# Optimization experiments

Hardware: AMD Instinct MI355X
Metric: run time of the kernel (lower is better)

## Reference

```python
import jax, jax.numpy as jnp
import numpy as np

HID = 256
EDGE_F = 64
N_CELL = 4096
N_EDGE = 65536
BSZ = 4
EPS = 1e-5


def setup_inputs() -> dict:
    key = jax.random.key(0)
    ks = jax.random.split(key, 12)
    def lin(k, fan_in, fan_out):
        # torch Linear default init: U(-1/sqrt(fan_in), 1/sqrt(fan_in))
        bound = 1.0 / np.sqrt(fan_in)
        kw, kb = jax.random.split(k)
        W = jax.random.uniform(kw, (fan_in, fan_out), jnp.float32, -bound, bound)
        b = jax.random.uniform(kb, (fan_out,), jnp.float32, -bound, bound)
        return W, b
    cell_x = jax.random.normal(ks[0], (BSZ, N_CELL, HID), jnp.float32)
    edge_index = jax.random.randint(ks[1], (BSZ, N_EDGE, 2), 0, N_CELL, jnp.int64)
    edge_attr = jax.random.normal(ks[2], (BSZ, N_EDGE, EDGE_F), jnp.float32)
    mW1, mb1 = lin(ks[3], HID + EDGE_F, HID)
    mW2, mb2 = lin(ks[4], HID, HID)
    uW1, ub1 = lin(ks[5], 2 * HID, HID)
    uW2, ub2 = lin(ks[6], HID, HID)
    gamma = jnp.ones((HID,), jnp.float32)
    beta = jnp.zeros((HID,), jnp.float32)
    return {"cell_x": cell_x, "edge_index": edge_index, "edge_attr": edge_attr,
            "mW1": mW1, "mb1": mb1, "mW2": mW2, "mb2": mb2,
            "uW1": uW1, "ub1": ub1, "uW2": uW2, "ub2": ub2,
            "gamma": gamma, "beta": beta}


def reference(cell_x, edge_index, edge_attr, mW1, mb1, mW2, mb2,
              uW1, ub1, uW2, ub2, gamma, beta):
    n_cell = cell_x.shape[1]
    src = jnp.clip(edge_index[..., 0], 0, n_cell - 1)  # [B, E]
    dst = jnp.clip(edge_index[..., 1], 0, n_cell - 1)  # [B, E]

    # gather source node features per edge: [B, E, H]
    src_x = jnp.take_along_axis(cell_x, src[..., None], axis=1)

    # edge message MLP
    m_in = jnp.concatenate([src_x, edge_attr], axis=-1)  # [B, E, H+F]
    msg = jax.nn.relu(m_in @ mW1 + mb1) @ mW2 + mb2      # [B, E, H]

    # mean aggregation at destination nodes (scatter-add + count)
    def agg_one(m, d):
        s = jax.ops.segment_sum(m, d, num_segments=n_cell)                    # [N, H]
        c = jax.ops.segment_sum(jnp.ones((d.shape[0],), m.dtype), d,
                                num_segments=n_cell)                          # [N]
        return s / jnp.maximum(c, 1.0)[:, None]
    agg = jax.vmap(agg_one)(msg, dst)  # [B, N, H]

    # node update MLP + residual LayerNorm
    u_in = jnp.concatenate([cell_x, agg], axis=-1)        # [B, N, 2H]
    out = jax.nn.relu(u_in @ uW1 + ub1) @ uW2 + ub2       # [B, N, H]
    h = cell_x + out
    mu = jnp.mean(h, axis=-1, keepdims=True)
    var = jnp.mean(jnp.square(h - mu), axis=-1, keepdims=True)
    return (h - mu) * jax.lax.rsqrt(var + EPS) * gamma + beta
```

## Files before the change

kernel.cpp:

```cpp
#include <hip/hip_runtime.h>
#include <hip/hip_bf16.h>

#define HID 256
#define EF  64
#define KIN 320
#define NC  4096
#define NE  65536
#define BSZ 4
#define EPSV 1e-5f

typedef unsigned short ushort_t;
typedef __attribute__((ext_vector_type(8))) short s16x8;
typedef __attribute__((ext_vector_type(16))) float f32x16;

#define EPAD 68
#define HPAD 260
#define UPAD 520
#define HSF  260

__device__ __forceinline__ ushort_t bf16_rne(float f) {
    unsigned u = __float_as_uint(f);
    return (ushort_t)((u + 0x7fffu + ((u >> 16) & 1u)) >> 16);
}
__device__ __forceinline__ float bf16_to_f(ushort_t u) {
    return __uint_as_float(((unsigned)u) << 16);
}
__device__ __forceinline__ unsigned pk_bf16(float a, float b) {
    __hip_bfloat162 h = __float22bfloat162_rn(make_float2(a, b));
    return *reinterpret_cast<unsigned*>(&h);
}
__device__ __forceinline__ void split_bf16(float v, ushort_t& h, ushort_t& l) {
    unsigned u = __float_as_uint(v);
    h = (ushort_t)(u >> 16);
    float hf = __uint_as_float(u & 0xffff0000u);
    l = (ushort_t)(__float_as_uint(v - hf) >> 16);
}

__device__ __forceinline__ void pack_one(const float* W, int idx,
                                         ushort_t* hi, ushort_t* lo) {
    int l = idx & 63;
    int tn = idx >> 6;
    int nt = tn & 7, t = tn >> 3;
    int k0 = t * 16 + (l >> 5) * 8;
    int col = nt * 32 + (l & 31);
    #pragma unroll
    for (int j = 0; j < 8; ++j) {
        float v = W[(size_t)(k0 + j) * 256 + col];
        ushort_t h, lw;
        split_bf16(v, h, lw);
        hi[(size_t)idx * 8 + j] = h;
        lo[(size_t)idx * 8 + j] = lw;
    }
}

#define FR1 10240
#define FR2 8192
#define PACK1B 104
#define FUSEB 256
#define ZEROB 256

__global__ __launch_bounds__(256)
void prep_kernel(const float* __restrict__ mW1, const float* __restrict__ uW1,
                 const float* __restrict__ uW2, const float* __restrict__ mW2,
                 const float* __restrict__ ub1, const float* __restrict__ mb2,
                 ushort_t* __restrict__ w1hi, ushort_t* __restrict__ w1lo,
                 ushort_t* __restrict__ u1hi, ushort_t* __restrict__ u1lo,
                 ushort_t* __restrict__ u2hi, ushort_t* __restrict__ u2lo,
                 float* __restrict__ W2u, float* __restrict__ bias2u,
                 float4* __restrict__ zp, int n4) {
    int bid = blockIdx.x;
    if (bid < PACK1B) {
        int idx = bid * 256 + threadIdx.x;
        if (idx < FR1) { pack_one(mW1, idx, w1hi, w1lo); return; }
        idx -= FR1;
        if (idx < FR2) { pack_one(uW1, idx, u1hi, u1lo); return; }
        idx -= FR2;
        pack_one(uW2, idx, u2hi, u2lo);
        return;
    }
    bid -= PACK1B;
    if (bid < FUSEB) {
        int k = bid, n = threadIdx.x;
        const float* wrow = mW2 + (size_t)k * 256;
        float acc = 0.f;
        #pragma unroll 8
        for (int m = 0; m < 256; ++m)
            acc = fmaf(wrow[m], uW1[(size_t)(256 + m) * 256 + n], acc);
        W2u[(size_t)k * 256 + n] = acc;
        return;
    }
    bid -= FUSEB;
    if (bid == 0) {
        int n = threadIdx.x;
        float acc = ub1[n];
        #pragma unroll 8
        for (int m = 0; m < 256; ++m)
            acc = fmaf(mb2[m], uW1[(size_t)(256 + m) * 256 + n], acc);
        bias2u[n] = acc;
        return;
    }
    bid -= 1;
    int i = bid * 256 + threadIdx.x;
    int stride = ZEROB * 256;
    float4 z = make_float4(0.f, 0.f, 0.f, 0.f);
    for (; i < n4; i += stride) zp[i] = z;
}

__global__ __launch_bounds__(512, 4)
void hp_kernel(const int* __restrict__ eidx, float* __restrict__ counts,
               const float* __restrict__ cell_x,
               const ushort_t* __restrict__ w1hi, const ushort_t* __restrict__ w1lo,
               const ushort_t* __restrict__ u1hi, const ushort_t* __restrict__ u1lo,
               float* __restrict__ Pe, ushort_t* __restrict__ Pn,
               const float* __restrict__ W2u,
               ushort_t* __restrict__ w2uhi, ushort_t* __restrict__ w2ulo) {
    __shared__ ushort_t Us[32 * HPAD];

    if (blockIdx.x < 512) {
        int i = blockIdx.x * 512 + threadIdx.x;
        int b = i >> 16;
        int2 v = ((const int2*)eidx)[i];
        int d = min(max(v.y, 0), NC - 1);
        atomicAdd(&counts[b * NC + d], 1.0f);
        return;
    }
    if (blockIdx.x >= 1024) {
        int idx = (blockIdx.x - 1024) * 512 + threadIdx.x;
        pack_one(W2u, idx, w2uhi, w2ulo);
        return;
    }

    const int tid = threadIdx.x;
    const size_t r0 = (size_t)(blockIdx.x - 512) * 32;
    const int wv = tid >> 6, ln = tid & 63;
    const int m32 = ln & 31, half = ln >> 5;
    const int col = wv * 32 + m32;

    const ushort_t* wph = w1hi + ((size_t)wv * 64 + ln) * 8;
    const ushort_t* wpl = w1lo + ((size_t)wv * 64 + ln) * 8;
    const ushort_t* uph = u1hi + ((size_t)wv * 64 + ln) * 8;
    const ushort_t* upl = u1lo + ((size_t)wv * 64 + ln) * 8;
    s16x8 wh = *(const s16x8*)wph, wl = *(const s16x8*)wpl;
    s16x8 uh = *(const s16x8*)uph, ul = *(const s16x8*)upl;

    {
        const int row = tid >> 4, c8 = tid & 15;
        const float4* crow = (const float4*)(cell_x + (r0 + row) * HID);
        #pragma unroll
        for (int i = 0; i < 4; ++i) {
            int c = c8 + i * 16;
            float4 v = crow[c];
            *(uint2*)&Us[row * HPAD + c * 4] =
                make_uint2(pk_bf16(v.x, v.y), pk_bf16(v.z, v.w));
        }
    }
    __syncthreads();

    f32x16 aw, au;
    #pragma unroll
    for (int r = 0; r < 16; ++r) { aw[r] = 0.f; au[r] = 0.f; }

    #pragma unroll 2
    for (int t = 0; t < 16; ++t) {
        int tn = (t + 1 < 16) ? t + 1 : 15;
        s16x8 whn = *(const s16x8*)(wph + (size_t)tn * 4096);
        s16x8 wln = *(const s16x8*)(wpl + (size_t)tn * 4096);
        s16x8 uhn = *(const s16x8*)(uph + (size_t)tn * 4096);
        s16x8 uln = *(const s16x8*)(upl + (size_t)tn * 4096);
        s16x8 a = *(const s16x8*)&Us[m32 * HPAD + t * 16 + half * 8];
        aw = __builtin_amdgcn_mfma_f32_32x32x16_bf16(a, wh, aw, 0, 0, 0);
        aw = __builtin_amdgcn_mfma_f32_32x32x16_bf16(a, wl, aw, 0, 0, 0);
        au = __builtin_amdgcn_mfma_f32_32x32x16_bf16(a, uh, au, 0, 0, 0);
        au = __builtin_amdgcn_mfma_f32_32x32x16_bf16(a, ul, au, 0, 0, 0);
        wh = whn; wl = wln; uh = uhn; ul = uln;
    }

    #pragma unroll
    for (int r = 0; r < 16; ++r) {
        int row = (r & 3) + 8 * (r >> 2) + 4 * half;
        Pe[(r0 + row) * 256 + col] = aw[r];
        Pn[(r0 + row) * 256 + col] = bf16_rne(au[r]);
    }
}

__global__ __launch_bounds__(512, 4)
void scansc_kernel(const int* __restrict__ eidx, const float* __restrict__ counts,
                   int* __restrict__ filled, int* __restrict__ sorted) {
    __shared__ int woffL[NC];
    __shared__ int wsum[8];

    const int t = threadIdx.x;
    const int b = blockIdx.x >> 7;

    int c[8];
    int ts = 0;
    const int base = b * NC + t * 8;
    #pragma unroll
    for (int j = 0; j < 8; ++j) { c[j] = (int)counts[base + j]; ts += c[j]; }

    int lane = t & 63;
    int x = ts;
    #pragma unroll
    for (int off = 1; off < 64; off <<= 1) {
        int y = __shfl_up(x, off, 64);
        if (lane >= off) x += y;
    }
    if (lane == 63) wsum[t >> 6] = x;
    __syncthreads();
    if (t == 0) {
        int s = 0;
        #pragma unroll
        for (int w = 0; w < 8; ++w) { int tmp = wsum[w]; wsum[w] = s; s += tmp; }
    }
    __syncthreads();
    int run = wsum[t >> 6] + (x - ts);
    #pragma unroll
    for (int j = 0; j < 8; ++j) { woffL[t * 8 + j] = run; run += c[j]; }
    __syncthreads();

    int e = (blockIdx.x & 127) * 512 + t;
    int2 v = ((const int2*)eidx)[(size_t)b * NE + e];
    int d = min(max(v.y, 0), NC - 1);
    int pos = woffL[d] + atomicAdd(&filled[b * NC + d], 1);
    sorted[(size_t)b * NE + pos] = e;
}

__global__ __launch_bounds__(512, 4)
void edge_kernel(const float* __restrict__ Pe,
                 const int*   __restrict__ eidx,
                 const int*   __restrict__ sorted,
                 const float* __restrict__ eattr,
                 const ushort_t* __restrict__ w1hi, const ushort_t* __restrict__ w1lo,
                 const float* __restrict__ b1,
                 float* __restrict__ aggf) {
    __shared__ ushort_t Xs[64 * EPAD];

    const int tid = threadIdx.x;
    const int b   = blockIdx.x >> 10;
    const int e0  = (blockIdx.x & 1023) * 64;
    const int wv = tid >> 6, ln = tid & 63;
    const int m32 = ln & 31, half = ln >> 5;
    const int col = wv * 32 + m32;

    int eid = sorted[(size_t)b * NE + e0 + ln];
    int2 ev = ((const int2*)eidx)[(size_t)b * NE + eid];
    int src = min(max(ev.x, 0), NC - 1);
    int dst = min(max(ev.y, 0), NC - 1);

    const ushort_t* ph = w1hi + ((size_t)(16 * 8 + wv) * 64 + ln) * 8;
    const ushort_t* pl = w1lo + ((size_t)(16 * 8 + wv) * 64 + ln) * 8;
    s16x8 bh0 = *(const s16x8*)ph;
    s16x8 bl0 = *(const s16x8*)pl;
    s16x8 bh1 = *(const s16x8*)(ph + 4096);
    s16x8 bl1 = *(const s16x8*)(pl + 4096);
    s16x8 bh2 = *(const s16x8*)(ph + 8192);
    s16x8 bl2 = *(const s16x8*)(pl + 8192);
    s16x8 bh3 = *(const s16x8*)(ph + 12288);
    s16x8 bl3 = *(const s16x8*)(pl + 12288);

    float t0[16], t1[16];
    {
        const float* pb = Pe + (size_t)b * NC * 256 + col;
        #pragma unroll
        for (int r = 0; r < 16; ++r) {
            int rw = (r & 3) + 8 * (r >> 2) + 4 * half;
            t0[r] = pb[(size_t)__shfl(src, rw, 64) * 256];
            t1[r] = pb[(size_t)__shfl(src, rw + 32, 64) * 256];
        }
    }

    {
        const int rowE = tid >> 3, c8 = tid & 7;
        int eidr = __shfl(eid, rowE, 64);
        const float4* arow = (const float4*)(eattr + ((size_t)b * NE + eidr) * EF);
        #pragma unroll
        for (int i = 0; i < 2; ++i) {
            int c = c8 + i * 8;
            float4 v = arow[c];
            *(uint2*)&Xs[rowE * EPAD + c * 4] =
                make_uint2(pk_bf16(v.x, v.y), pk_bf16(v.z, v.w));
        }
    }
    __syncthreads();

    f32x16 A0, A1;
    {
        float bias = b1[col];
        #pragma unroll
        for (int r = 0; r < 16; ++r) { A0[r] = bias; A1[r] = bias; }
    }
    {
        int ao = m32 * EPAD + half * 8;
        s16x8 a0, a1;
        a0 = *(const s16x8*)&Xs[ao];      a1 = *(const s16x8*)&Xs[ao + 32 * EPAD];
        A0 = __builtin_amdgcn_mfma_f32_32x32x16_bf16(a0, bh0, A0, 0, 0, 0);
        A0 = __builtin_amdgcn_mfma_f32_32x32x16_bf16(a0, bl0, A0, 0, 0, 0);
        A1 = __builtin_amdgcn_mfma_f32_32x32x16_bf16(a1, bh0, A1, 0, 0, 0);
        A1 = __builtin_amdgcn_mfma_f32_32x32x16_bf16(a1, bl0, A1, 0, 0, 0);
        a0 = *(const s16x8*)&Xs[ao + 16]; a1 = *(const s16x8*)&Xs[ao + 16 + 32 * EPAD];
        A0 = __builtin_amdgcn_mfma_f32_32x32x16_bf16(a0, bh1, A0, 0, 0, 0);
        A0 = __builtin_amdgcn_mfma_f32_32x32x16_bf16(a0, bl1, A0, 0, 0, 0);
        A1 = __builtin_amdgcn_mfma_f32_32x32x16_bf16(a1, bh1, A1, 0, 0, 0);
        A1 = __builtin_amdgcn_mfma_f32_32x32x16_bf16(a1, bl1, A1, 0, 0, 0);
        a0 = *(const s16x8*)&Xs[ao + 32]; a1 = *(const s16x8*)&Xs[ao + 32 + 32 * EPAD];
        A0 = __builtin_amdgcn_mfma_f32_32x32x16_bf16(a0, bh2, A0, 0, 0, 0);
        A0 = __builtin_amdgcn_mfma_f32_32x32x16_bf16(a0, bl2, A0, 0, 0, 0);
        A1 = __builtin_amdgcn_mfma_f32_32x32x16_bf16(a1, bh2, A1, 0, 0, 0);
        A1 = __builtin_amdgcn_mfma_f32_32x32x16_bf16(a1, bl2, A1, 0, 0, 0);
        a0 = *(const s16x8*)&Xs[ao + 48]; a1 = *(const s16x8*)&Xs[ao + 48 + 32 * EPAD];
        A0 = __builtin_amdgcn_mfma_f32_32x32x16_bf16(a0, bh3, A0, 0, 0, 0);
        A0 = __builtin_amdgcn_mfma_f32_32x32x16_bf16(a0, bl3, A0, 0, 0, 0);
        A1 = __builtin_amdgcn_mfma_f32_32x32x16_bf16(a1, bh3, A1, 0, 0, 0);
        A1 = __builtin_amdgcn_mfma_f32_32x32x16_bf16(a1, bl3, A1, 0, 0, 0);
    }

    #pragma unroll
    for (int r = 0; r < 16; ++r) {
        A0[r] = fmaxf(A0[r] + t0[r], 0.f);
        A1[r] = fmaxf(A1[r] + t1[r], 0.f);
    }

    {
        const int l31 = ln & 31;
        int dl = __shfl(dst, l31, 64);
        int dp = __shfl(dst, (l31 == 0) ? 0 : l31 - 1, 64);
        if (l31 == 0) dp = ~dl;
        unsigned m = (unsigned)__ballot(dl != dp);
        unsigned rem = m & ~1u;
        float prev = (((A0[0] + A0[1]) + (A0[2] + A0[3])) + ((A0[4] + A0[5]) + (A0[6] + A0[7])))
                   + (((A0[8] + A0[9]) + (A0[10] + A0[11])) + ((A0[12] + A0[13]) + (A0[14] + A0[15])));
        int lo = 0;
        while (lo < 32) {
            int hi = rem ? (int)__builtin_ctz(rem) : 32;
            rem &= rem - 1;
            int d = __shfl(dl, lo, 64);
            float shi = 0.f;
            if (hi < 32) {
                #pragma unroll
                for (int r = 0; r < 16; ++r) {
                    int row = (r & 3) + 8 * (r >> 2) + 4 * half;
                    shi += (row >= hi) ? A0[r] : 0.f;
                }
            }
            float s = prev - shi;
            prev = shi;
            s += __shfl_xor(s, 32, 64);
            if (ln < 32) atomicAdd(&aggf[((size_t)b * NC + d) * HID + col], s);
            lo = hi;
        }
        dl = __shfl(dst, 32 + l31, 64);
        dp = __shfl(dst, 32 + ((l31 == 0) ? 0 : l31 - 1), 64);
        if (l31 == 0) dp = ~dl;
        m = (unsigned)__ballot(dl != dp);
        rem = m & ~1u;
        prev = (((A1[0] + A1[1]) + (A1[2] + A1[3])) + ((A1[4] + A1[5]) + (A1[6] + A1[7])))
             + (((A1[8] + A1[9]) + (A1[10] + A1[11])) + ((A1[12] + A1[13]) + (A1[14] + A1[15])));
        lo = 0;
        while (lo < 32) {
            int hi = rem ? (int)__builtin_ctz(rem) : 32;
            rem &= rem - 1;
            int d = __shfl(dl, lo, 64);
            float shi = 0.f;
            if (hi < 32) {
                #pragma unroll
                for (int r = 0; r < 16; ++r) {
                    int row = (r & 3) + 8 * (r >> 2) + 4 * half;
                    shi += (row >= hi) ? A1[r] : 0.f;
                }
            }
            float s = prev - shi;
            prev = shi;
            s += __shfl_xor(s, 32, 64);
            if (ln < 32) atomicAdd(&aggf[((size_t)b * NC + d) * HID + col], s);
            lo = hi;
        }
    }
}

__global__ __launch_bounds__(512, 6)
void node_kernel(const float* __restrict__ cell_x,
                 const float* __restrict__ aggf,
                 const float* __restrict__ counts,
                 const ushort_t* __restrict__ Pn,
                 const ushort_t* __restrict__ w2uhi, const ushort_t* __restrict__ w2ulo,
                 const float* __restrict__ bias2u,
                 const ushort_t* __restrict__ u2hi, const ushort_t* __restrict__ u2lo,
                 const float* __restrict__ b2,
                 const float* __restrict__ gamma, const float* __restrict__ beta,
                 float* __restrict__ out) {
    __shared__ ushort_t Us[32 * UPAD];
    float* hs = (float*)Us;

    const int tid = threadIdx.x;
    const int b   = blockIdx.x >> 7;
    const int r0  = (blockIdx.x & 127) * 32;
    const int wv = tid >> 6, ln = tid & 63;
    const int m32 = ln & 31, half = ln >> 5;
    const int col = wv * 32 + m32;

    const ushort_t* b1ph = w2uhi + ((size_t)wv * 64 + ln) * 8;
    const ushort_t* b1pl = w2ulo + ((size_t)wv * 64 + ln) * 8;
    s16x8 bhi = *(const s16x8*)b1ph;
    s16x8 blo = *(const s16x8*)b1pl;

    ushort_t pnt[16];
    {
        const ushort_t* pb = Pn + ((size_t)b * NC + r0) * 256 + col;
        #pragma unroll
        for (int r = 0; r < 16; ++r) {
            int row = (r & 3) + 8 * (r >> 2) + 4 * half;
            pnt[r] = pb[(size_t)row * 256];
        }
    }

    {
        const int row = tid >> 4, c8 = tid & 15;
        float inv = 1.0f / fmaxf(counts[b * NC + r0 + row], 1.0f);
        const float4* grow = (const float4*)(aggf + ((size_t)b * NC + r0 + row) * HID);
        #pragma unroll
        for (int i = 0; i < 4; ++i) {
            int c = c8 + i * 16;
            float4 g = grow[c];
            *(uint2*)&Us[row * HPAD + c * 4] =
                make_uint2(pk_bf16(g.x * inv, g.y * inv), pk_bf16(g.z * inv, g.w * inv));
        }
    }
    __syncthreads();

    f32x16 acc;
    {
        float bias = bias2u[col];
        #pragma unroll
        for (int r = 0; r < 16; ++r) acc[r] = bias;
    }
    #pragma unroll 2
    for (int t = 0; t < 16; ++t) {
        int tn1 = (t + 1 < 16) ? t + 1 : 15;
        s16x8 bhin = *(const s16x8*)(b1ph + (size_t)tn1 * 4096);
        s16x8 blon = *(const s16x8*)(b1pl + (size_t)tn1 * 4096);
        s16x8 a = *(const s16x8*)&Us[m32 * HPAD + t * 16 + half * 8];
        acc = __builtin_amdgcn_mfma_f32_32x32x16_bf16(a, bhi, acc, 0, 0, 0);
        acc = __builtin_amdgcn_mfma_f32_32x32x16_bf16(a, blo, acc, 0, 0, 0);
        bhi = bhin; blo = blon;
    }

    #pragma unroll
    for (int r = 0; r < 16; ++r) acc[r] += bf16_to_f(pnt[r]);

    const ushort_t* b2ph = u2hi + ((size_t)wv * 64 + ln) * 8;
    const ushort_t* b2pl = u2lo + ((size_t)wv * 64 + ln) * 8;
    bhi = *(const s16x8*)b2ph;
    blo = *(const s16x8*)b2pl;

    __syncthreads();

    #pragma unroll
    for (int r = 0; r < 16; ++r) {
        int row = (r & 3) + 8 * (r >> 2) + 4 * half;
        Us[row * HPAD + col] = bf16_rne(fmaxf(acc[r], 0.f));
    }
    __syncthreads();

    float cxt[16];
    #pragma unroll
    for (int r = 0; r < 16; ++r) {
        int row = (r & 3) + 8 * (r >> 2) + 4 * half;
        cxt[r] = cell_x[((size_t)b * NC + r0 + row) * HID + col];
    }

    f32x16 c2;
    {
        float bias = b2[col];
        #pragma unroll
        for (int r = 0; r < 16; ++r) c2[r] = bias;
    }
    #pragma unroll 2
    for (int t = 0; t < 16; ++t) {
        int tn1 = (t + 1 < 16) ? t + 1 : 15;
        s16x8 bhin = *(const s16x8*)(b2ph + (size_t)tn1 * 4096);
        s16x8 blon = *(const s16x8*)(b2pl + (size_t)tn1 * 4096);
        s16x8 a = *(const s16x8*)&Us[m32 * HPAD + t * 16 + half * 8];
        c2 = __builtin_amdgcn_mfma_f32_32x32x16_bf16(a, bhi, c2, 0, 0, 0);
        c2 = __builtin_amdgcn_mfma_f32_32x32x16_bf16(a, blo, c2, 0, 0, 0);
        bhi = bhin; blo = blon;
    }
    __syncthreads();

    #pragma unroll
    for (int r = 0; r < 16; ++r) {
        int row = (r & 3) + 8 * (r >> 2) + 4 * half;
        hs[row * HSF + col] = c2[r] + cxt[r];
    }
    __syncthreads();

    #pragma unroll
    for (int i = 0; i < 4; ++i) {
        int r = wv * 4 + i;
        float v[4];
        float s = 0.f, q = 0.f;
        #pragma unroll
        for (int j = 0; j < 4; ++j) {
            v[j] = hs[r * HSF + ln + 64 * j];
            s += v[j];
            q = fmaf(v[j], v[j], q);
        }
        #pragma unroll
        for (int off = 32; off > 0; off >>= 1) {
            s += __shfl_xor(s, off, 64);
            q += __shfl_xor(q, off, 64);
        }
        float mu = s * (1.0f / HID);
        float var = q * (1.0f / HID) - mu * mu;
        float rs = rsqrtf(var + EPSV);
        float* orow = out + ((size_t)b * NC + r0 + r) * HID;
        #pragma unroll
        for (int j = 0; j < 4; ++j) {
            int c = ln + 64 * j;
            orow[c] = (v[j] - mu) * rs * gamma[c] + beta[c];
        }
    }
}

extern "C" void kernel_launch(void* const* d_in, const int* in_sizes, int n_in,
                              void* d_out, int out_size, void* d_ws, size_t ws_size,
                              hipStream_t stream) {
    const float* cell_x = (const float*)d_in[0];
    const int*   eidx   = (const int*)d_in[1];
    const float* eattr  = (const float*)d_in[2];
    const float* mW1    = (const float*)d_in[3];
    const float* mb1    = (const float*)d_in[4];
    const float* mW2    = (const float*)d_in[5];
    const float* mb2    = (const float*)d_in[6];
    const float* uW1    = (const float*)d_in[7];
    const float* ub1    = (const float*)d_in[8];
    const float* uW2    = (const float*)d_in[9];
    const float* ub2    = (const float*)d_in[10];
    const float* gamma  = (const float*)d_in[11];
    const float* beta   = (const float*)d_in[12];
    float* out = (float*)d_out;

    float* aggf   = (float*)d_ws;
    float* counts = aggf + (size_t)BSZ * NC * HID;
    int*   filled = (int*)(counts + BSZ * NC);
    int*   sorted = filled + BSZ * NC;
    ushort_t* w1hi = (ushort_t*)(sorted + (size_t)BSZ * NE);
    ushort_t* w1lo = w1hi + KIN * HID;
    ushort_t* u1hi = w1lo + KIN * HID;
    ushort_t* u1lo = u1hi + HID * HID;
    ushort_t* u2hi = u1lo + HID * HID;
    ushort_t* u2lo = u2hi + HID * HID;
    ushort_t* w2uhi = u2lo + HID * HID;
    ushort_t* w2ulo = w2uhi + HID * HID;
    float*    W2u   = (float*)(w2ulo + HID * HID);
    float*    bias2u = W2u + HID * HID;
    float*    Pe   = bias2u + HID;
    ushort_t* Pn   = (ushort_t*)(Pe + (size_t)BSZ * NC * 256);

    int n4 = (BSZ * NC * HID * 4 + BSZ * NC * 4 + BSZ * NC * 4) / 16;
    prep_kernel<<<PACK1B + FUSEB + 1 + ZEROB, 256, 0, stream>>>(
        mW1, uW1, uW2, mW2, ub1, mb2,
        w1hi, w1lo, u1hi, u1lo, u2hi, u2lo, W2u, bias2u, (float4*)d_ws, n4);
    hp_kernel<<<1040, 512, 0, stream>>>(eidx, counts, cell_x,
                                        w1hi, w1lo, u1hi, u1lo, Pe, Pn,
                                        W2u, w2uhi, w2ulo);
    scansc_kernel<<<512, 512, 0, stream>>>(eidx, counts, filled, sorted);
    edge_kernel<<<BSZ * NE / 64, 512, 0, stream>>>(Pe, eidx, sorted, eattr,
                                                   w1hi, w1lo, mb1, aggf);
    node_kernel<<<BSZ * NC / 32, 512, 0, stream>>>(cell_x, aggf, counts, Pn,
                                                   w2uhi, w2ulo, bias2u,
                                                   u2hi, u2lo, ub2,
                                                   gamma, beta, out);
}
```

Measured before the change: 251.2 us.

## Fold scan-scatter into hp kernel, move histogram to prep, use memset

Measured after the change: 249.0 us. No clear change (-0.9%).

```diff
diff --git a/kernel.cpp b/kernel.cpp
--- a/kernel.cpp
+++ b/kernel.cpp
@@ -17,6 +17,7 @@
 #define HPAD 260
 #define UPAD 520
 #define HSF  260
+#define HOFF 8320
 
 __device__ __forceinline__ ushort_t bf16_rne(float f) {
     unsigned u = __float_as_uint(f);
@@ -57,7 +58,7 @@
 #define FR2 8192
 #define PACK1B 104
 #define FUSEB 256
-#define ZEROB 256
+#define HISTB 1024
 
 __global__ __launch_bounds__(256)
 void prep_kernel(const float* __restrict__ mW1, const float* __restrict__ uW1,
@@ -67,7 +68,7 @@
                  ushort_t* __restrict__ u1hi, ushort_t* __restrict__ u1lo,
                  ushort_t* __restrict__ u2hi, ushort_t* __restrict__ u2lo,
                  float* __restrict__ W2u, float* __restrict__ bias2u,
-                 float4* __restrict__ zp, int n4) {
+                 const int* __restrict__ eidx, float* __restrict__ counts) {
     int bid = blockIdx.x;
     if (bid < PACK1B) {
         int idx = bid * 256 + threadIdx.x;
@@ -101,13 +102,15 @@
     }
     bid -= 1;
     int i = bid * 256 + threadIdx.x;
-    int stride = ZEROB * 256;
-    float4 z = make_float4(0.f, 0.f, 0.f, 0.f);
-    for (; i < n4; i += stride) zp[i] = z;
+    int b = i >> 16;
+    int2 v = ((const int2*)eidx)[i];
+    int d = min(max(v.y, 0), NC - 1);
+    atomicAdd(&counts[b * NC + d], 1.0f);
 }
 
 __global__ __launch_bounds__(512, 4)
-void hp_kernel(const int* __restrict__ eidx, float* __restrict__ counts,
+void hp_kernel(const int* __restrict__ eidx, const float* __restrict__ counts,
+               int* __restrict__ filled, int* __restrict__ sorted,
                const float* __restrict__ cell_x,
                const ushort_t* __restrict__ w1hi, const ushort_t* __restrict__ w1lo,
                const ushort_t* __restrict__ u1hi, const ushort_t* __restrict__ u1lo,
@@ -115,23 +118,56 @@
                const float* __restrict__ W2u,
                ushort_t* __restrict__ w2uhi, ushort_t* __restrict__ w2ulo) {
     __shared__ ushort_t Us[32 * HPAD];
-
-    if (blockIdx.x < 512) {
-        int i = blockIdx.x * 512 + threadIdx.x;
-        int b = i >> 16;
-        int2 v = ((const int2*)eidx)[i];
-        int d = min(max(v.y, 0), NC - 1);
-        atomicAdd(&counts[b * NC + d], 1.0f);
-        return;
-    }
+    __shared__ int wsum[8];
+
     if (blockIdx.x >= 1024) {
         int idx = (blockIdx.x - 1024) * 512 + threadIdx.x;
         pack_one(W2u, idx, w2uhi, w2ulo);
         return;
     }
 
+    if (blockIdx.x >= 512) {
+        int* woffL = (int*)Us;
+        const int t = threadIdx.x;
+        const int sbid = blockIdx.x - 512;
+        const int b = sbid >> 7;
+
+        int c[8];
+        int ts = 0;
+        const int base = b * NC + t * 8;
+        #pragma unroll
+        for (int j = 0; j < 8; ++j) { c[j] = (int)counts[base + j]; ts += c[j]; }
+
+        int lane = t & 63;
+        int x = ts;
+        #pragma unroll
+        for (int off = 1; off < 64; off <<= 1) {
+            int y = __shfl_up(x, off, 64);
+            if (lane >= off) x += y;
+        }
+        if (lane == 63) wsum[t >> 6] = x;
+        __syncthreads();
+        if (t == 0) {
+            int s = 0;
+            #pragma unroll
+            for (int w = 0; w < 8; ++w) { int tmp = wsum[w]; wsum[w] = s; s += tmp; }
+        }
+        __syncthreads();
+        int run = wsum[t >> 6] + (x - ts);
+        #pragma unroll
+        for (int j = 0; j < 8; ++j) { woffL[t * 8 + j] = run; run += c[j]; }
+        __syncthreads();
+
+        int e = (sbid & 127) * 512 + t;
+        int2 v = ((const int2*)eidx)[(size_t)b * NE + e];
+        int d = min(max(v.y, 0), NC - 1);
+        int pos = woffL[d] + atomicAdd(&filled[b * NC + d], 1);
+        sorted[(size_t)b * NE + pos] = e;
+        return;
+    }
+
     const int tid = threadIdx.x;
-    const size_t r0 = (size_t)(blockIdx.x - 512) * 32;
+    const size_t r0 = (size_t)blockIdx.x * 32;
     const int wv = tid >> 6, ln = tid & 63;
     const int m32 = ln & 31, half = ln >> 5;
     const int col = wv * 32 + m32;
@@ -181,48 +217,6 @@
         Pe[(r0 + row) * 256 + col] = aw[r];
         Pn[(r0 + row) * 256 + col] = bf16_rne(au[r]);
     }
-}
-
-__global__ __launch_bounds__(512, 4)
-void scansc_kernel(const int* __restrict__ eidx, const float* __restrict__ counts,
-                   int* __restrict__ filled, int* __restrict__ sorted) {
-    __shared__ int woffL[NC];
-    __shared__ int wsum[8];
-
-    const int t = threadIdx.x;
-    const int b = blockIdx.x >> 7;
-
-    int c[8];
-    int ts = 0;
-    const int base = b * NC + t * 8;
-    #pragma unroll
-    for (int j = 0; j < 8; ++j) { c[j] = (int)counts[base + j]; ts += c[j]; }
-
-    int lane = t & 63;
-    int x = ts;
-    #pragma unroll
-    for (int off = 1; off < 64; off <<= 1) {
-        int y = __shfl_up(x, off, 64);
-        if (lane >= off) x += y;
-    }
-    if (lane == 63) wsum[t >> 6] = x;
-    __syncthreads();
-    if (t == 0) {
-        int s = 0;
-        #pragma unroll
-        for (int w = 0; w < 8; ++w) { int tmp = wsum[w]; wsum[w] = s; s += tmp; }
-    }
-    __syncthreads();
-    int run = wsum[t >> 6] + (x - ts);
-    #pragma unroll
-    for (int j = 0; j < 8; ++j) { woffL[t * 8 + j] = run; run += c[j]; }
-    __syncthreads();
-
-    int e = (blockIdx.x & 127) * 512 + t;
-    int2 v = ((const int2*)eidx)[(size_t)b * NE + e];
-    int d = min(max(v.y, 0), NC - 1);
-    int pos = woffL[d] + atomicAdd(&filled[b * NC + d], 1);
-    sorted[(size_t)b * NE + pos] = e;
 }
 
 __global__ __launch_bounds__(512, 4)
@@ -377,7 +371,7 @@
     }
 }
 
-__global__ __launch_bounds__(512, 6)
+__global__ __launch_bounds__(512, 4)
 void node_kernel(const float* __restrict__ cell_x,
                  const float* __restrict__ aggf,
                  const float* __restrict__ counts,
@@ -452,12 +446,10 @@
     bhi = *(const s16x8*)b2ph;
     blo = *(const s16x8*)b2pl;
 
-    __syncthreads();
-
     #pragma unroll
     for (int r = 0; r < 16; ++r) {
         int row = (r & 3) + 8 * (r >> 2) + 4 * half;
-        Us[row * HPAD + col] = bf16_rne(fmaxf(acc[r], 0.f));
+        Us[HOFF + row * HPAD + col] = bf16_rne(fmaxf(acc[r], 0.f));
     }
     __syncthreads();
 
@@ -479,7 +471,7 @@
         int tn1 = (t + 1 < 16) ? t + 1 : 15;
         s16x8 bhin = *(const s16x8*)(b2ph + (size_t)tn1 * 4096);
         s16x8 blon = *(const s16x8*)(b2pl + (size_t)tn1 * 4096);
-        s16x8 a = *(const s16x8*)&Us[m32 * HPAD + t * 16 + half * 8];
+        s16x8 a = *(const s16x8*)&Us[HOFF + m32 * HPAD + t * 16 + half * 8];
         c2 = __builtin_amdgcn_mfma_f32_32x32x16_bf16(a, bhi, c2, 0, 0, 0);
         c2 = __builtin_amdgcn_mfma_f32_32x32x16_bf16(a, blo, c2, 0, 0, 0);
         bhi = bhin; blo = blon;
@@ -556,14 +548,15 @@
     float*    Pe   = bias2u + HID;
     ushort_t* Pn   = (ushort_t*)(Pe + (size_t)BSZ * NC * 256);
 
-    int n4 = (BSZ * NC * HID * 4 + BSZ * NC * 4 + BSZ * NC * 4) / 16;
-    prep_kernel<<<PACK1B + FUSEB + 1 + ZEROB, 256, 0, stream>>>(
+    size_t zbytes = (size_t)BSZ * NC * HID * 4 + (size_t)BSZ * NC * 4 + (size_t)BSZ * NC * 4;
+    hipMemsetAsync(d_ws, 0, zbytes, stream);
+
+    prep_kernel<<<PACK1B + FUSEB + 1 + HISTB, 256, 0, stream>>>(
         mW1, uW1, uW2, mW2, ub1, mb2,
-        w1hi, w1lo, u1hi, u1lo, u2hi, u2lo, W2u, bias2u, (float4*)d_ws, n4);
-    hp_kernel<<<1040, 512, 0, stream>>>(eidx, counts, cell_x,
+        w1hi, w1lo, u1hi, u1lo, u2hi, u2lo, W2u, bias2u, eidx, counts);
+    hp_kernel<<<1040, 512, 0, stream>>>(eidx, counts, filled, sorted, cell_x,
                                         w1hi, w1lo, u1hi, u1lo, Pe, Pn,
                                         W2u, w2uhi, w2ulo);
-    scansc_kernel<<<512, 512, 0, stream>>>(eidx, counts, filled, sorted);
     edge_kernel<<<BSZ * NE / 64, 512, 0, stream>>>(Pe, eidx, sorted, eattr,
                                                    w1hi, w1lo, mb1, aggf);
     node_kernel<<<BSZ * NC / 32, 512, 0, stream>>>(cell_x, aggf, counts, Pn,
```
